# Kernel tuning notes

Measured on AMD Instinct MI355X. Metric: run time of the kernel, lower is better.

## Reference

```python
import jax, jax.numpy as jnp
import numpy as np

D_MODEL = 2048
NUM_GROUPS = 16
D_HEAD = D_MODEL // NUM_GROUPS
ROTARY_DIM = int(D_MODEL * 0.25)  # 512


def setup_inputs() -> dict:
    key = jax.random.key(0)
    ks = jax.random.split(key, 8)
    B, S, N = 4, 2048, 2048
    scale = 1.0 / np.sqrt(D_MODEL)
    return {
        "query": jax.random.normal(ks[0], (B, S, D_MODEL), jnp.float32),
        "key": jax.random.normal(ks[1], (B, N, D_MODEL), jnp.float32),
        "value": jax.random.normal(ks[2], (B, N, D_MODEL), jnp.float32),
        "mask": jax.random.randint(ks[3], (B, S), 0, 2, jnp.int32),
        "position_ids": jnp.arange(S, dtype=jnp.int64) if jax.config.jax_enable_x64 else jnp.arange(S, dtype=jnp.int32),
        "Wq": jax.random.normal(ks[4], (D_MODEL, D_MODEL), jnp.float32) * scale,
        "Wk": jax.random.normal(ks[5], (D_MODEL, D_MODEL), jnp.float32) * scale,
        "Wv": jax.random.normal(ks[6], (D_MODEL, D_MODEL), jnp.float32) * scale,
        "Wo": jax.random.normal(ks[7], (D_MODEL, D_MODEL), jnp.float32) * scale,
    }


def _apply_rope_query_only(q, k, position_ids):
    # Faithful to source: rotary embedding is applied to query ONLY; key is returned unchanged.
    rd = ROTARY_DIM
    pos = position_ids.astype(q.dtype)  # (S,)
    freq = jnp.arange(0, rd, 2, dtype=q.dtype)
    inv_freq = 1.0 / (10000.0 ** (freq / rd))  # (rd/2,)
    pe = pos[:, None] * inv_freq[None, :]       # (S, rd/2)
    cos = jnp.tile(jnp.cos(pe), (1, 2))[None]   # (1, S, rd) tiled [c, c]
    sin = jnp.tile(jnp.sin(pe), (1, 2))[None]
    q_rot, q_pass = q[..., :rd], q[..., rd:]
    half = rd // 2
    q_rot_half = jnp.concatenate([-q_rot[..., half:], q_rot[..., :half]], axis=-1)
    q_rot = q_rot * cos + q_rot_half * sin
    q = jnp.concatenate([q_rot, q_pass], axis=-1)
    return q, k


def reference(query, key, value, mask, position_ids, Wq, Wk, Wv, Wo):
    B, S, _ = query.shape
    N = key.shape[1]
    G, dh = NUM_GROUPS, D_HEAD

    q = query @ Wq.T
    k = key @ Wk.T
    v = value @ Wv.T

    q, k = _apply_rope_query_only(q, k, position_ids)

    qh = q.reshape(B, S, G, dh).transpose(0, 2, 1, 3)  # (B,G,S,dh)
    kh = k.reshape(B, N, G, dh).transpose(0, 2, 1, 3)  # (B,G,N,dh)
    vh = v.reshape(B, N, G, dh).transpose(0, 2, 1, 3)  # (B,G,N,dh)

    scores = jnp.einsum("bgsd,bgnd->bgsn", qh, kh) / jnp.sqrt(jnp.asarray(dh, q.dtype))
    # mask (B,S) -> (B,1,1,N); here S == N so pad width is 0 (pad value 1 in source)
    m = mask[:, None, None, :]
    scores = jnp.where(m == 0, -jnp.inf, scores)

    w = jax.nn.softmax(scores, axis=-1)
    out = jnp.einsum("bgsn,bgnd->bgsd", w, vh)           # (B,G,S,dh)
    out = out.transpose(0, 2, 1, 3).reshape(B, S, D_MODEL)
    return out @ Wo.T
```

## Files before the change

### kernel.cpp

```cpp
#include <hip/hip_runtime.h>
#include <hip/hip_bf16.h>
#include <type_traits>
#include <utility>

typedef unsigned short u16;
typedef unsigned int u32;
typedef __attribute__((ext_vector_type(8))) short  s16x8;
typedef __attribute__((ext_vector_type(4))) short  s16x4;
typedef __attribute__((ext_vector_type(4))) float  f32x4;
typedef __attribute__((ext_vector_type(16))) float f32x16;
typedef __bf16 bf16x8_t __attribute__((ext_vector_type(8)));
typedef __bf16 bf16x2_t __attribute__((ext_vector_type(2)));

#define SEQ 2048
#define DMODEL 2048
#define NBATCH 4
#define DH 128
#define NB (NBATCH * SEQ)
#define EMAX 40

#define QK_SCALE_LOG2 0.12754375f
#define BIAS_VALID  (-34.624681f)
#define BIAS_MASKED (-180.0f)

#if __has_builtin(__builtin_amdgcn_exp2f)
#define EXP2(x) __builtin_amdgcn_exp2f(x)
#else
#define EXP2(x) exp2f(x)
#endif

#define BARRIER __builtin_amdgcn_s_barrier()
#define FENCE  asm volatile("" ::: "memory")
#define LGKM0  asm volatile("s_waitcnt lgkmcnt(0)" ::: "memory")
#define VMCNT4 asm volatile("s_waitcnt vmcnt(4)" ::: "memory")
#define VMCNT0 asm volatile("s_waitcnt vmcnt(0)" ::: "memory")

static __device__ __forceinline__ u16 f2bf(float f) {
  unsigned u = __float_as_uint(f);
  u += 0x7fffu + ((u >> 16) & 1u);
  return (u16)(u >> 16);
}
static __device__ __forceinline__ float bf2f(u16 h) {
  return __uint_as_float(((unsigned)h) << 16);
}
static __device__ __forceinline__ u32 pack_bf16(float a, float b) {
  bf16x2_t t; t[0] = (__bf16)a; t[1] = (__bf16)b;
  return __builtin_bit_cast(u32, t);
}
static __device__ __forceinline__ void plswap(u32& a, u32& b) {
  asm("v_permlane32_swap_b32 %0, %1" : "+v"(a), "+v"(b));
}

template <typename T, typename = void>
struct mfma_takes : std::false_type {};
template <typename T>
struct mfma_takes<T, std::void_t<decltype(__builtin_amdgcn_mfma_f32_16x16x32_bf16(
    std::declval<T>(), std::declval<T>(), std::declval<f32x4>(), 0, 0, 0))>>
    : std::true_type {};
using mfma_frag_t = std::conditional_t<mfma_takes<s16x8>::value, s16x8, bf16x8_t>;

static __device__ __forceinline__ f32x16 mfma32(s16x8 a, s16x8 b, f32x16 c) {
  return __builtin_amdgcn_mfma_f32_32x32x16_bf16(
      __builtin_bit_cast(mfma_frag_t, a), __builtin_bit_cast(mfma_frag_t, b), c, 0, 0, 0);
}

typedef const void __attribute__((address_space(1)))* gas_ptr;
typedef void __attribute__((address_space(3)))* las_ptr;
static __device__ __forceinline__ void gload16(const void* g, void* l) {
  __builtin_amdgcn_global_load_lds((gas_ptr)g, (las_ptr)l, 16, 0, 0);
}

static __device__ __forceinline__ s16x8 frag_from_words(u32 w0, u32 w1, u32 w2, u32 w3) {
  union { u32 w[4]; s16x8 v; } u;
  u.w[0] = w0; u.w[1] = w1; u.w[2] = w2; u.w[3] = w3;
  return u.v;
}

static __device__ __forceinline__ void cvt8(const float* src, u16* dst, int i) {
  const float4* p = (const float4*)src + (size_t)i * 2;
  float4 a = p[0], b4 = p[1];
  s16x8 o;
  o[0] = (short)f2bf(a.x);  o[1] = (short)f2bf(a.y);
  o[2] = (short)f2bf(a.z);  o[3] = (short)f2bf(a.w);
  o[4] = (short)f2bf(b4.x); o[5] = (short)f2bf(b4.y);
  o[6] = (short)f2bf(b4.z); o[7] = (short)f2bf(b4.w);
  *(s16x8*)(dst + (size_t)i * 8) = o;
}

__global__ void cvt1_k(const float* __restrict__ in, u16* __restrict__ out, int n8) {
  const int stride = (int)(gridDim.x * blockDim.x);
  for (int i = (int)(blockIdx.x * blockDim.x + threadIdx.x); i < n8; i += stride)
    cvt8(in, out, i);
}

__global__ void cvt4_k(const float* __restrict__ a, const float* __restrict__ b,
                       const float* __restrict__ c, const float* __restrict__ d,
                       u16* __restrict__ oa, u16* __restrict__ ob,
                       u16* __restrict__ oc, u16* __restrict__ od) {
  const int n8 = 1 << 19;
  const int stride = (int)(gridDim.x * blockDim.x);
  for (int i = (int)(blockIdx.x * blockDim.x + threadIdx.x); i < 4 * n8; i += stride) {
    const int seg = i >> 19, off = i & (n8 - 1);
    const float* src = seg == 0 ? a : (seg == 1 ? b : (seg == 2 ? c : d));
    u16* dst = seg == 0 ? oa : (seg == 1 ? ob : (seg == 2 ? oc : od));
    cvt8(src, dst, off);
  }
}

__global__ void scan_k(const int* __restrict__ mask, int* __restrict__ idx,
                       u16* __restrict__ biasc, int* __restrict__ meta) {
  __shared__ int nv_sh[4];
  const int tid = (int)threadIdx.x;
  const int w = tid >> 6, lane = tid & 63;
  const int* mb = mask + w * SEQ;
  int cnt = 0;
  for (int it = 0; it < SEQ / 64; ++it) {
    const int i = it * 64 + lane;
    const bool m = mb[i] != 0;
    const unsigned long long bal = __ballot(m);
    const int pos = cnt + __popcll(bal & ((1ull << lane) - 1ull));
    if (m) idx[w * SEQ + pos] = i;
    cnt += __popcll(bal);
  }
  if (lane == 0) nv_sh[w] = cnt;
  __syncthreads();
  const int nv = nv_sh[w];
  const int npad = (nv + 255) & ~255;
  for (int j = nv + lane; j < npad; j += 64) idx[w * SEQ + j] = 0;
  for (int j = lane; j < SEQ; j += 64)
    biasc[w * SEQ + j] = (j < nv) ? f2bf(BIAS_VALID) : f2bf(BIAS_MASKED);
  if (tid == 0) {
    int off = 0;
    for (int b2 = 0; b2 < 4; ++b2) {
      const int nvb = nv_sh[b2];
      meta[b2] = off;
      meta[4 + b2] = (nvb + 63) >> 6;
      off += (nvb + 255) & ~255;
    }
    meta[8] = off;
  }
}

__global__ void gathercvt_k(const float* __restrict__ keyf,
                            const float* __restrict__ valf,
                            const int* __restrict__ idx, const int* __restrict__ meta,
                            u16* __restrict__ xkc, u16* __restrict__ xvc) {
  const int b = (int)blockIdx.y;
  const int j = (int)blockIdx.x;
  const int mstart = meta[b];
  const int mend = (b < 3) ? meta[b + 1] : meta[8];
  if (mstart + j >= mend) return;
  const int src = idx[b * SEQ + j];
  const float* ks = keyf + ((size_t)b * SEQ + src) * DMODEL;
  const float* vs = valf + ((size_t)b * SEQ + src) * DMODEL;
  u16* kd = xkc + (size_t)(mstart + j) * DMODEL;
  u16* vd = xvc + (size_t)(mstart + j) * DMODEL;
  cvt8(ks, kd, (int)threadIdx.x);
  cvt8(vs, vd, (int)threadIdx.x);
}

static __device__ void gemm_body(const u16* __restrict__ A, const u16* __restrict__ Bw,
                                 void* __restrict__ Cv, const int outmode,
                                 const int bm, const int bn, const int mlimit,
                                 const int kt0, const int ntl) {
  constexpr int M = 8192, N = 2048, K = 2048;
  __shared__ u16 Ab[2][256 * 64];
  __shared__ u16 Bb[2][256 * 64];

  if (bm * 256 >= mlimit) return;

  const int tid = (int)threadIdx.x;
  const int wv = tid >> 6, lane = tid & 63;
  const int l32 = lane & 31, hi = lane >> 5;
  const int wm = wv >> 2, wn = wv & 3;

  const size_t arow0 = (size_t)bm * 256;
  const size_t brow0 = (size_t)bn * 256;

  const int srow = tid >> 3;
  const int scolb = (tid & 7) * 16;
  const int scol = (scolb ^ ((srow & 7) << 4)) >> 1;
  const u16* agp = A  + (arow0 + srow) * (size_t)K + scol;
  const u16* bgp = Bw + (brow0 + srow) * (size_t)K + scol;

  f32x16 acc[4][2];
#pragma unroll
  for (int mi = 0; mi < 4; ++mi)
#pragma unroll
    for (int ni = 0; ni < 2; ++ni)
#pragma unroll
      for (int r = 0; r < 16; ++r) acc[mi][ni][r] = 0.f;

  auto SH_A = [&](int kt2, u16* bufA, int half) {
#pragma unroll
    for (int j = 0; j < 2; ++j) {
      const int rb = half * 128 + j * 64;
      gload16(agp + (size_t)rb * K + kt2, bufA + (rb + wv * 8) * 64);
    }
  };
  auto SH_B = [&](int kt2, u16* bufB, int half) {
#pragma unroll
    for (int j = 0; j < 2; ++j) {
      const int rb = half * 128 + j * 64;
      gload16(bgp + (size_t)rb * K + kt2, bufB + (rb + wv * 8) * 64);
    }
  };
  auto LDA = [&](const u16* buf, int qm, s16x8* af) {
#pragma unroll
    for (int mb = 0; mb < 2; ++mb) {
      const int row = wm * 128 + qm * 64 + mb * 32 + l32;
#pragma unroll
      for (int ks = 0; ks < 4; ++ks) {
        const int cb = ((ks * 32 + hi * 16) ^ ((row & 7) << 4)) >> 1;
        af[mb * 4 + ks] = *(const s16x8*)&buf[row * 64 + cb];
      }
    }
  };
  auto LDB = [&](const u16* buf, int qn, s16x8* bfr) {
    const int row = wn * 64 + qn * 32 + l32;
#pragma unroll
    for (int ks = 0; ks < 4; ++ks) {
      const int cb = ((ks * 32 + hi * 16) ^ ((row & 7) << 4)) >> 1;
      bfr[ks] = *(const s16x8*)&buf[row * 64 + cb];
    }
  };
  auto MM = [&](const s16x8* af, const s16x8* bfr, int qm, int qn) {
    __builtin_amdgcn_s_setprio(1);
#pragma unroll
    for (int mb = 0; mb < 2; ++mb)
#pragma unroll
      for (int ks = 0; ks < 4; ++ks)
        acc[qm * 2 + mb][qn] = mfma32(af[mb * 4 + ks], bfr[ks], acc[qm * 2 + mb][qn]);
    __builtin_amdgcn_s_setprio(0);
  };

  SH_A(kt0, Ab[0], 0); SH_A(kt0, Ab[0], 1);
  SH_B(kt0, Bb[0], 0); SH_B(kt0, Bb[0], 1);
  SH_B(kt0 + 64, Bb[1], 0); SH_B(kt0 + 64, Bb[1], 1);
  VMCNT4; BARRIER;

  for (int t = 0; t < ntl; ++t) {
    u16* Ac = Ab[t & 1];
    u16* Bc = Bb[t & 1];
    u16* An = Ab[(t + 1) & 1];
    u16* Bn = Bb[t & 1];
    const int kA = kt0 + (t + 1) * 64;
    const int kB = kt0 + (t + 2) * 64;
    const bool stA = (t + 1 < ntl);
    const bool stB = (t + 2 < ntl);
    s16x8 af0[8], af1[8], bf0[4], bf1[4];

    LDA(Ac, 0, af0); LDB(Bc, 0, bf0);
    if (stA) SH_A(kA, An, 0);
    BARRIER; LGKM0;
    MM(af0, bf0, 0, 0);
    BARRIER;
    LDB(Bc, 1, bf1);
    if (stA) SH_A(kA, An, 1);
    BARRIER; LGKM0;
    MM(af0, bf1, 0, 1);
    BARRIER;
    LDA(Ac, 1, af1);
    if (stB) SH_B(kB, Bn, 0);
    BARRIER; LGKM0;
    MM(af1, bf1, 1, 1);
    BARRIER;
    if (stB) { SH_B(kB, Bn, 1); VMCNT4; }
    else if (stA) { VMCNT0; }
    BARRIER; LGKM0;
    MM(af1, bf0, 1, 0);
    BARRIER;
  }

  const size_t row0 = arow0 + (size_t)wm * 128;
  const size_t col0 = brow0 + (size_t)wn * 64;
  if (outmode == 0) {
    u16* C = (u16*)Cv;
#pragma unroll
    for (int mi = 0; mi < 4; ++mi)
#pragma unroll
      for (int ni = 0; ni < 2; ++ni) {
        const size_t rbase = row0 + mi * 32 + 4 * hi;
        const size_t c = col0 + ni * 32 + l32;
#pragma unroll
        for (int q = 0; q < 4; ++q)
#pragma unroll
          for (int rr = 0; rr < 4; ++rr)
            C[(rbase + 8 * q + rr) * N + c] = f2bf(acc[mi][ni][q * 4 + rr]);
      }
  } else if (outmode == 1) {
    float* C = (float*)Cv;
#pragma unroll
    for (int mi = 0; mi < 4; ++mi)
#pragma unroll
      for (int ni = 0; ni < 2; ++ni) {
        const size_t rbase = row0 + mi * 32 + 4 * hi;
        const size_t c = col0 + ni * 32 + l32;
#pragma unroll
        for (int q = 0; q < 4; ++q)
#pragma unroll
          for (int rr = 0; rr < 4; ++rr)
            C[(rbase + 8 * q + rr) * N + c] = acc[mi][ni][q * 4 + rr];
      }
  } else if (outmode == 3) {
    float* S = (float*)Cv;
#pragma unroll
    for (int mi = 0; mi < 4; ++mi)
#pragma unroll
      for (int ni = 0; ni < 2; ++ni) {
        const int rb = wm * 128 + mi * 32 + 4 * hi;
        const int cl = wn * 64 + ni * 32 + l32;
#pragma unroll
        for (int q = 0; q < 4; ++q)
#pragma unroll
          for (int rr = 0; rr < 4; ++rr)
            atomicAdd(&S[(rb + 8 * q + rr) * 256 + cl], acc[mi][ni][q * 4 + rr]);
      }
  } else {
    u16* T = &Ab[0][0];
    constexpr int RS = 264;
    u16* C = (u16*)Cv;
    for (int c = 0; c < 4; ++c) {
      BARRIER;
      if (wn == c) {
#pragma unroll
        for (int mi = 0; mi < 4; ++mi)
#pragma unroll
          for (int ni = 0; ni < 2; ++ni) {
            const int tok0 = wm * 128 + mi * 32 + 4 * hi;
            const int dc = ni * 32 + l32;
#pragma unroll
            for (int q = 0; q < 4; ++q) {
              s16x4 v;
#pragma unroll
              for (int rr = 0; rr < 4; ++rr) v[rr] = (short)f2bf(acc[mi][ni][q * 4 + rr]);
              *(s16x4*)&T[dc * RS + tok0 + 8 * q] = v;
            }
          }
      }
      BARRIER;
      const int dr = tid >> 3, tc = tid & 7;
      u16* dst = C + (brow0 + c * 64 + dr) * (size_t)M + arow0 + tc * 32;
      const u16* srcT = &T[dr * RS + tc * 32];
#pragma unroll
      for (int v4 = 0; v4 < 4; ++v4)
        *(s16x8*)(dst + v4 * 8) = *(const s16x8*)(srcT + v4 * 8);
    }
    BARRIER;
  }
}

__global__ __launch_bounds__(512, 2) void gemmfused_k(
    const u16* __restrict__ xq, const u16* __restrict__ wq, u16* __restrict__ qout,
    const u16* __restrict__ xkc, const u16* __restrict__ wk, u16* __restrict__ kout,
    const u16* __restrict__ xvc, const u16* __restrict__ wv, u16* __restrict__ vtout,
    const int* __restrict__ meta, float* __restrict__ scratch) {
  const int Mc = meta[8];
  const int T = Mc >> 8;
  int e = 16 * T - 256;
  if (e < 0) e = 0;
  if (e > EMAX) e = EMAX;
  const int nkf = 8 * T - e;
  const int qstart = nkf + 8 * T;
  const int b = (int)blockIdx.x;

  if (b < nkf) {
    gemm_body(xkc, wk, (void*)kout, 0, b >> 3, b & 7, Mc, 0, 32);
  } else if (b < qstart) {
    const int i = b - nkf;
    gemm_body(xvc, wv, (void*)vtout, 2, i >> 3, i & 7, Mc, 0, 32);
  } else if (b < qstart + 256) {
    const int i = b - qstart;
    gemm_body(xq, wq, (void*)qout, 0, i >> 3, i & 7, 8192, 0, 32);
  } else if (b >= 768 && b < 768 + 2 * e) {
    const int j = b - 768;
    const int o = j >> 1, half = j & 1;
    const int idx = nkf + o;
    gemm_body(xkc, wk, (void*)(scratch + (size_t)o * 65536), 3,
              idx >> 3, idx & 7, Mc, half * 1024, 16);
  }
}

__global__ void fixup_k(u16* __restrict__ kout, const float* __restrict__ scratch,
                        const int* __restrict__ meta) {
  const int o = (int)blockIdx.y;
  const int Mc = meta[8];
  const int T = Mc >> 8;
  int e = 16 * T - 256;
  if (e < 0) e = 0;
  if (e > EMAX) e = EMAX;
  if (o >= e) return;
  const int nkf = 8 * T - e;
  const int idx = nkf + o;
  const int bm = idx >> 3, bn = idx & 7;
  const int r = (int)blockIdx.x;
  const int c = (int)threadIdx.x;
  kout[((size_t)bm * 256 + r) * DMODEL + bn * 256 + c] =
      f2bf(scratch[(size_t)o * 65536 + r * 256 + c]);
}

__global__ __launch_bounds__(512, 2) void gemmwo_k(const u16* __restrict__ A,
                                                   const u16* __restrict__ Bw,
                                                   float* __restrict__ C) {
  const int bid = (int)blockIdx.x;
  const int bn = (bid >> 3) & 7;
  const int bm = (bid & 7) * 4 + (bid >> 6);
  gemm_body(A, Bw, (void*)C, 1, bm, bn, 8192, 0, 32);
}

__global__ void rope_k(u16* __restrict__ qb, const int* __restrict__ pos_ids) {
  const int row = (int)blockIdx.x;
  const int s = row & (SEQ - 1);
  const int t = (int)threadIdx.x;
  const float pos = (float)pos_ids[s];
  const float ang = pos * exp2f((float)t * (-13.287712379549449f / 256.0f));
  float sn, cs;
  sincosf(ang, &sn, &cs);
  u16* p = qb + (size_t)row * DMODEL;
  const float x = bf2f(p[t]);
  const float y = bf2f(p[t + 256]);
  p[t]       = f2bf((x * cs - y * sn) * QK_SCALE_LOG2);
  p[t + 256] = f2bf((y * cs + x * sn) * QK_SCALE_LOG2);
#pragma unroll
  for (int j = 0; j < 6; ++j) {
    const int d = 512 + t + 256 * j;
    p[d] = f2bf(bf2f(p[d]) * QK_SCALE_LOG2);
  }
}

__device__ __forceinline__ void attn_stage(u16* Ks, u16* Vs,
                                           const u16* kbase, const u16* vbase,
                                           int kt, int w, int lane) {
#pragma unroll
  for (int i = 0; i < 4; ++i) {
    const int row = w * 16 + i * 4 + (lane >> 4);
    const int srcb = ((lane & 15) * 16) ^ ((row & 7) << 4);
    gload16(kbase + (size_t)(kt + row) * DMODEL + (srcb >> 1), &Ks[(w * 16 + i * 4) * 128]);
  }
#pragma unroll
  for (int i = 0; i < 4; ++i) {
    const int row = w * 32 + i * 8 + (lane >> 3);
    const int srcb = ((lane & 7) * 16) ^ ((row & 7) << 4);
    gload16(vbase + (size_t)row * NB + kt + (srcb >> 1), &Vs[(w * 32 + i * 8) * 64]);
  }
}

__global__ __launch_bounds__(256) void attn_k(const u16* __restrict__ q,
                                              const u16* __restrict__ kc,
                                              const u16* __restrict__ vtc,
                                              const u16* __restrict__ biasc,
                                              const int* __restrict__ meta,
                                              u16* __restrict__ att) {
  __shared__ u16 Ks[2][64 * 128];
  __shared__ u16 Vs[2][128 * 64];

  const int tid = (int)threadIdx.x;
  const int w = tid >> 6, lane = tid & 63;
  const int l32 = lane & 31, hi = lane >> 5;

  const int bid = (int)blockIdx.x;
  const int sb = (bid & 7) * 128 + (bid >> 3);
  const int qt = sb & 15;
  const int bg = sb >> 4;
  const int b = bg >> 4, g = bg & 15;

  const int mstart = meta[b];
  const int nt = meta[4 + b];

  const int qrow = qt * 128 + w * 32 + l32;
  const u16* qp = q + ((size_t)b * SEQ + qrow) * DMODEL + g * DH;
  s16x8 aq[8];
#pragma unroll
  for (int s = 0; s < 8; ++s) aq[s] = *(const s16x8*)(qp + s * 16 + hi * 8);

  const u32 one0 = (hi == 0) ? 0x00003F80u : 0u;
  const s16x8 bones = frag_from_words(one0, 0, 0, 0);
  const s16x8 allones = frag_from_words(0x3F803F80u, 0x3F803F80u, 0x3F803F80u, 0x3F803F80u);

  f32x16 oacc[4], lacc;
#pragma unroll
  for (int r = 0; r < 16; ++r) {
    lacc[r] = 0.f;
#pragma unroll
    for (int d0 = 0; d0 < 4; ++d0) oacc[d0][r] = 0.f;
  }

  const u16* kbase = kc + (size_t)mstart * DMODEL + g * DH;
  const u16* vbase = vtc + (size_t)(g * DH) * NB + mstart;
  const u16* bbase = biasc + b * SEQ;

  attn_stage(Ks[0], Vs[0], kbase, vbase, 0, w, lane);
  u16 bb0 = bbase[l32], bb1 = bbase[32 + l32];

  for (int t = 0; t < nt; ++t) {
    const int cur = t & 1;
    __syncthreads();
    u16 bbn0 = bb0, bbn1 = bb1;
    if (t < nt - 1) {
      attn_stage(Ks[cur ^ 1], Vs[cur ^ 1], kbase, vbase, (t + 1) * 64, w, lane);
      bbn0 = bbase[(t + 1) * 64 + l32];
      bbn1 = bbase[(t + 1) * 64 + 32 + l32];
    }
    const u16* KsC = Ks[cur];
    const u16* VsC = Vs[cur];

    const s16x8 ab0 = frag_from_words((hi == 0) ? (u32)bb0 : 0u, 0, 0, 0);
    const s16x8 ab1 = frag_from_words((hi == 0) ? (u32)bb1 : 0u, 0, 0, 0);
    __builtin_amdgcn_s_setprio(1);
    f32x16 sacc0 = mfma32(ab0, bones, (f32x16)(0.f));
    f32x16 sacc1 = mfma32(ab1, bones, (f32x16)(0.f));

#pragma unroll
    for (int s = 0; s < 8; ++s) {
      const int byteoff = ((s * 32 + hi * 16) ^ ((l32 & 7) << 4)) >> 1;
      const s16x8 a0 = *(const s16x8*)&KsC[l32 * 128 + byteoff];
      const s16x8 a1 = *(const s16x8*)&KsC[(32 + l32) * 128 + byteoff];
      sacc0 = mfma32(a0, aq[s], sacc0);
      sacc1 = mfma32(a1, aq[s], sacc1);
    }
    __builtin_amdgcn_s_setprio(0);

    u32 pk0[8], pk1[8];
#pragma unroll
    for (int i = 0; i < 8; ++i) {
      pk0[i] = pack_bf16(EXP2(sacc0[2 * i]), EXP2(sacc0[2 * i + 1]));
      pk1[i] = pack_bf16(EXP2(sacc1[2 * i]), EXP2(sacc1[2 * i + 1]));
    }
    s16x8 pa[4];
#pragma unroll
    for (int grp = 0; grp < 4; ++grp) {
      u32* pk = (grp < 2) ? pk0 : pk1;
      const int o = (grp & 1) * 4;
      plswap(pk[o + 0], pk[o + 2]);
      plswap(pk[o + 1], pk[o + 3]);
      pa[grp] = frag_from_words(pk[o + 0], pk[o + 1], pk[o + 2], pk[o + 3]);
    }

    __builtin_amdgcn_s_setprio(1);
#pragma unroll
    for (int ks = 0; ks < 4; ++ks) lacc = mfma32(pa[ks], allones, lacc);

#pragma unroll
    for (int d0 = 0; d0 < 4; ++d0) {
      const int rowd = d0 * 32 + l32;
#pragma unroll
      for (int ks = 0; ks < 4; ++ks) {
        const int byteoff = ((ks * 32 + hi * 16) ^ ((rowd & 7) << 4)) >> 1;
        const s16x8 bv = *(const s16x8*)&VsC[rowd * 64 + byteoff];
        oacc[d0] = mfma32(pa[ks], bv, oacc[d0]);
      }
    }
    __builtin_amdgcn_s_setprio(0);
    bb0 = bbn0; bb1 = bbn1;
  }

  float rinv[16];
#pragma unroll
  for (int r = 0; r < 16; ++r) rinv[r] = 1.0f / lacc[r];
  u16* ob = att + ((size_t)b * SEQ + qt * 128 + w * 32) * DMODEL + g * DH;
#pragma unroll
  for (int d0 = 0; d0 < 4; ++d0)
#pragma unroll
    for (int r = 0; r < 16; ++r) {
      const int qloc = (r & 3) + 8 * (r >> 2) + 4 * hi;
      ob[(size_t)qloc * DMODEL + d0 * 32 + l32] = f2bf(oacc[d0][r] * rinv[r]);
    }
}

extern "C" void kernel_launch(void* const* d_in, const int* in_sizes, int n_in,
                              void* d_out, int out_size, void* d_ws, size_t ws_size,
                              hipStream_t stream) {
  const float* query = (const float*)d_in[0];
  const float* key   = (const float*)d_in[1];
  const float* value = (const float*)d_in[2];
  const int*   maskp = (const int*)d_in[3];
  const int*   posp  = (const int*)d_in[4];
  const float* Wq    = (const float*)d_in[5];
  const float* Wk    = (const float*)d_in[6];
  const float* Wv    = (const float*)d_in[7];
  const float* Wo    = (const float*)d_in[8];

  char* ws = (char*)d_ws;
  const size_t MB = 1024ull * 1024ull;
  u16* wq_b = (u16*)(ws + 0 * MB);
  u16* wk_b = (u16*)(ws + 8 * MB);
  u16* wv_b = (u16*)(ws + 16 * MB);
  u16* wo_b = (u16*)(ws + 24 * MB);
  u16* xq   = (u16*)(ws + 32 * MB);
  u16* xkc  = (u16*)(ws + 64 * MB);
  u16* xvc  = (u16*)(ws + 96 * MB);
  u16* qb   = (u16*)(ws + 128 * MB);
  u16* kc   = (u16*)(ws + 160 * MB);
  u16* vtc  = (u16*)(ws + 192 * MB);
  float* scratch = (float*)(ws + 160 * MB + (size_t)5376 * DMODEL * 2);
  char* aux = ws + 224 * MB;
  int* meta  = (int*)aux;
  int* idx   = (int*)(aux + 256);
  u16* biasc = (u16*)(aux + 256 + 32768);
  u16* att   = xq;

  hipMemsetAsync(scratch, 0, (size_t)EMAX * 65536 * 4, stream);
  scan_k<<<dim3(1), dim3(256), 0, stream>>>(maskp, idx, biasc, meta);
  cvt1_k<<<dim3(2048), dim3(256), 0, stream>>>(query, xq, (NBATCH * SEQ * DMODEL) / 8);
  gathercvt_k<<<dim3(SEQ, NBATCH), dim3(256), 0, stream>>>(key, value, idx, meta, xkc, xvc);
  cvt4_k<<<dim3(1024), dim3(256), 0, stream>>>(Wq, Wk, Wv, Wo, wq_b, wk_b, wv_b, wo_b);

  gemmfused_k<<<dim3(768 + 2 * EMAX), dim3(512), 0, stream>>>(
      xq, wq_b, qb, xkc, wk_b, kc, xvc, wv_b, vtc, meta, scratch);
  fixup_k<<<dim3(256, EMAX), dim3(256), 0, stream>>>(kc, scratch, meta);

  rope_k<<<dim3(NBATCH * SEQ), dim3(256), 0, stream>>>(qb, posp);

  attn_k<<<dim3(1024), dim3(256), 0, stream>>>(qb, kc, vtc, biasc, meta, att);

  gemmwo_k<<<dim3(256), dim3(512), 0, stream>>>(att, wo_b, (float*)d_out);

  (void)in_sizes; (void)n_in; (void)out_size; (void)ws_size;
}
```

Before: 548.9 us.

## Restructure fused QKV GEMM scheduling, shrink split-K, and merge conversion kernels

The fused Q/K/V projection kernel gets a fixed 544-block grid. The first 32 blocks do the split-K tail tiles of K, now capped at 16 and disabled when the compacted length exceeds 5120. The next 256 blocks each compute one K tile followed by one V tile, with V visited in reversed row order. The rest compute Q tiles, using a swizzled block-to-tile mapping intended to improve L2 reuse. The separate query and weight fp32-to-bf16 conversion kernels are merged into one launch. V tiles are now issued for every row block regardless of the compacted length, which may add wasted work or out-of-range tiles.

```diff
diff --git a/kernel.cpp b/kernel.cpp
--- a/kernel.cpp
+++ b/kernel.cpp
@@ -17,7 +17,7 @@
 #define NBATCH 4
 #define DH 128
 #define NB (NBATCH * SEQ)
-#define EMAX 40
+#define ESPLIT 16
 
 #define QK_SCALE_LOG2 0.12754375f
 #define BIAS_VALID  (-34.624681f)
@@ -30,7 +30,6 @@
 #endif
 
 #define BARRIER __builtin_amdgcn_s_barrier()
-#define FENCE  asm volatile("" ::: "memory")
 #define LGKM0  asm volatile("s_waitcnt lgkmcnt(0)" ::: "memory")
 #define VMCNT4 asm volatile("s_waitcnt vmcnt(4)" ::: "memory")
 #define VMCNT0 asm volatile("s_waitcnt vmcnt(0)" ::: "memory")
@@ -87,23 +86,24 @@
   *(s16x8*)(dst + (size_t)i * 8) = o;
 }
 
-__global__ void cvt1_k(const float* __restrict__ in, u16* __restrict__ out, int n8) {
+__global__ void cvtall_k(const float* __restrict__ q, const float* __restrict__ a,
+                         const float* __restrict__ b, const float* __restrict__ c,
+                         const float* __restrict__ d, u16* __restrict__ oq,
+                         u16* __restrict__ oa, u16* __restrict__ ob,
+                         u16* __restrict__ oc, u16* __restrict__ od) {
+  const int nq = 1 << 21, nw = 1 << 19;
+  const int total = nq + 4 * nw;
   const int stride = (int)(gridDim.x * blockDim.x);
-  for (int i = (int)(blockIdx.x * blockDim.x + threadIdx.x); i < n8; i += stride)
-    cvt8(in, out, i);
-}
-
-__global__ void cvt4_k(const float* __restrict__ a, const float* __restrict__ b,
-                       const float* __restrict__ c, const float* __restrict__ d,
-                       u16* __restrict__ oa, u16* __restrict__ ob,
-                       u16* __restrict__ oc, u16* __restrict__ od) {
-  const int n8 = 1 << 19;
-  const int stride = (int)(gridDim.x * blockDim.x);
-  for (int i = (int)(blockIdx.x * blockDim.x + threadIdx.x); i < 4 * n8; i += stride) {
-    const int seg = i >> 19, off = i & (n8 - 1);
-    const float* src = seg == 0 ? a : (seg == 1 ? b : (seg == 2 ? c : d));
-    u16* dst = seg == 0 ? oa : (seg == 1 ? ob : (seg == 2 ? oc : od));
-    cvt8(src, dst, off);
+  for (int i = (int)(blockIdx.x * blockDim.x + threadIdx.x); i < total; i += stride) {
+    if (i < nq) {
+      cvt8(q, oq, i);
+    } else {
+      const int j = i - nq;
+      const int seg = j >> 19, off = j & (nw - 1);
+      const float* src = seg == 0 ? a : (seg == 1 ? b : (seg == 2 ? c : d));
+      u16* dst = seg == 0 ? oa : (seg == 1 ? ob : (seg == 2 ? oc : od));
+      cvt8(src, dst, off);
+    }
   }
 }
 
@@ -139,6 +139,14 @@
     }
     meta[8] = off;
   }
+}
+
+static __device__ __forceinline__ int calc_e(int Mc) {
+  if (Mc > 5120) return 0;
+  int e = 16 * (Mc >> 8) - 256;
+  if (e < 0) e = 0;
+  if (e > ESPLIT) e = ESPLIT;
+  return e;
 }
 
 __global__ void gathercvt_k(const float* __restrict__ keyf,
@@ -357,27 +365,28 @@
     const int* __restrict__ meta, float* __restrict__ scratch) {
   const int Mc = meta[8];
   const int T = Mc >> 8;
-  int e = 16 * T - 256;
-  if (e < 0) e = 0;
-  if (e > EMAX) e = EMAX;
-  const int nkf = 8 * T - e;
-  const int qstart = nkf + 8 * T;
-  const int b = (int)blockIdx.x;
-
-  if (b < nkf) {
-    gemm_body(xkc, wk, (void*)kout, 0, b >> 3, b & 7, Mc, 0, 32);
-  } else if (b < qstart) {
-    const int i = b - nkf;
-    gemm_body(xvc, wv, (void*)vtout, 2, i >> 3, i & 7, Mc, 0, 32);
-  } else if (b < qstart + 256) {
-    const int i = b - qstart;
-    gemm_body(xq, wq, (void*)qout, 0, i >> 3, i & 7, 8192, 0, 32);
-  } else if (b >= 768 && b < 768 + 2 * e) {
-    const int j = b - 768;
-    const int o = j >> 1, half = j & 1;
-    const int idx = nkf + o;
-    gemm_body(xkc, wk, (void*)(scratch + (size_t)o * 65536), 3,
-              idx >> 3, idx & 7, Mc, half * 1024, 16);
+  const int e = calc_e(Mc);
+  const int bid = (int)blockIdx.x;
+
+  if (bid < 32) {
+    const int o = bid >> 1, half = bid & 1;
+    if (o < e) {
+      const int kt = 8 * T - e + o;
+      gemm_body(xkc, wk, (void*)(scratch + (size_t)o * 65536), 3,
+                kt >> 3, kt & 7, Mc, half * 1024, 16);
+    }
+  } else if (bid < 288) {
+    const int g = bid - 32;
+    const int bn = (g >> 3) & 7;
+    const int bm = (g & 7) * 4 + (g >> 6);
+    if (bm * 8 + bn < 8 * T - e)
+      gemm_body(xkc, wk, (void*)kout, 0, bm, bn, Mc, 0, 32);
+    gemm_body(xvc, wv, (void*)vtout, 2, 31 - bm, bn, Mc, 0, 32);
+  } else {
+    const int g = bid - 288;
+    const int bn = (g >> 3) & 7;
+    const int bm = (g & 7) * 4 + (g >> 6);
+    gemm_body(xq, wq, (void*)qout, 0, bm, bn, 8192, 0, 32);
   }
 }
 
@@ -386,13 +395,10 @@
   const int o = (int)blockIdx.y;
   const int Mc = meta[8];
   const int T = Mc >> 8;
-  int e = 16 * T - 256;
-  if (e < 0) e = 0;
-  if (e > EMAX) e = EMAX;
+  const int e = calc_e(Mc);
   if (o >= e) return;
-  const int nkf = 8 * T - e;
-  const int idx = nkf + o;
-  const int bm = idx >> 3, bn = idx & 7;
+  const int kt = 8 * T - e + o;
+  const int bm = kt >> 3, bn = kt & 7;
   const int r = (int)blockIdx.x;
   const int c = (int)threadIdx.x;
   kout[((size_t)bm * 256 + r) * DMODEL + bn * 256 + c] =
@@ -599,15 +605,15 @@
   u16* biasc = (u16*)(aux + 256 + 32768);
   u16* att   = xq;
 
-  hipMemsetAsync(scratch, 0, (size_t)EMAX * 65536 * 4, stream);
+  hipMemsetAsync(scratch, 0, (size_t)ESPLIT * 65536 * 4, stream);
   scan_k<<<dim3(1), dim3(256), 0, stream>>>(maskp, idx, biasc, meta);
-  cvt1_k<<<dim3(2048), dim3(256), 0, stream>>>(query, xq, (NBATCH * SEQ * DMODEL) / 8);
+  cvtall_k<<<dim3(3072), dim3(256), 0, stream>>>(query, Wq, Wk, Wv, Wo,
+                                                 xq, wq_b, wk_b, wv_b, wo_b);
   gathercvt_k<<<dim3(SEQ, NBATCH), dim3(256), 0, stream>>>(key, value, idx, meta, xkc, xvc);
-  cvt4_k<<<dim3(1024), dim3(256), 0, stream>>>(Wq, Wk, Wv, Wo, wq_b, wk_b, wv_b, wo_b);
-
-  gemmfused_k<<<dim3(768 + 2 * EMAX), dim3(512), 0, stream>>>(
+
+  gemmfused_k<<<dim3(544), dim3(512), 0, stream>>>(
       xq, wq_b, qb, xkc, wk_b, kc, xvc, wv_b, vtc, meta, scratch);
-  fixup_k<<<dim3(256, EMAX), dim3(256), 0, stream>>>(kc, scratch, meta);
+  fixup_k<<<dim3(256, ESPLIT), dim3(256), 0, stream>>>(kc, scratch, meta);
 
   rope_k<<<dim3(NBATCH * SEQ), dim3(256), 0, stream>>>(qb, posp);
 
```

Measured after the change: 545.4 us. No clear change (-0.6%).
